# Optimization experiments

Measured on AMD Instinct MI355X. Metric: run time of the kernel, lower is better.

Reference implementation:

```python
import jax, jax.numpy as jnp
import numpy as np

B, Nq, C, H = 1, 300, 256, 8
h, w = 32, 32
HW = h * w
HID = 512  # rpe_hidden_dim
HD = C // H


def setup_inputs() -> dict:
    key = jax.random.key(0)
    ks = jax.random.split(key, 16)
    s = 0.02
    inp = {
        "raw_query": jax.random.normal(ks[0], (B, Nq, C), jnp.float32),
        "query_pos": jax.random.normal(ks[1], (B, Nq, C), jnp.float32),
        "reference_points": jax.random.uniform(ks[2], (B, Nq, 2), jnp.float32),
        "raw_src": jax.random.normal(ks[3], (B, HW, C), jnp.float32),
        "src_pos_embed": jax.random.normal(ks[4], (B, HW, C), jnp.float32),
        "Wq": jax.random.normal(ks[5], (C, C), jnp.float32) * s,
        "bq": jnp.zeros((C,), jnp.float32),
        "Wk": jax.random.normal(ks[6], (C, C), jnp.float32) * s,
        "bk": jnp.zeros((C,), jnp.float32),
        "Wv": jax.random.normal(ks[7], (C, C), jnp.float32) * s,
        "bv": jnp.zeros((C,), jnp.float32),
        "Wo": jax.random.normal(ks[8], (C, C), jnp.float32) * s,
        "bo": jnp.zeros((C,), jnp.float32),
        "W1": jax.random.normal(ks[9], (HID, 2), jnp.float32),   # cpb MLP layer 1
        "b1": jnp.zeros((HID,), jnp.float32),
        "W2": jax.random.normal(ks[10], (H, HID), jnp.float32) * s,  # cpb MLP layer 2 (no bias)
        "input_spatial_shapes": np.array([[h, w]], dtype=np.int64),
    }
    return inp


def _key_positions(hh, ww):
    ys = (jnp.arange(hh, dtype=jnp.float32) + 0.5) / hh
    xs = (jnp.arange(ww, dtype=jnp.float32) + 0.5) / ww
    yy, xx = jnp.meshgrid(ys, xs, indexing="ij")  # row-major: idx = y*w + x
    return jnp.stack([xx.ravel(), yy.ravel()], axis=-1)  # [HW, 2] (x, y)


def reference(raw_query, query_pos, reference_points, raw_src, src_pos_embed,
              Wq, bq, Wk, bk, Wv, bv, Wo, bo, W1, b1, W2, input_spatial_shapes):
    hh, ww = int(input_spatial_shapes[0, 0]), int(input_spatial_shapes[0, 1])
    scale = HD ** (-0.5)
    queries = raw_query + query_pos                      # [B,Nq,C]
    memory = raw_src + src_pos_embed                     # [B,HW,C]

    q = (queries @ Wq.T + bq).reshape(B, Nq, H, HD)
    k = (memory @ Wk.T + bk).reshape(B, hh * ww, H, HD)
    v = (memory @ Wv.T + bv).reshape(B, hh * ww, H, HD)

    logits = jnp.einsum("bqhd,bkhd->bhqk", q, k) * scale  # [B,H,Nq,HW]

    key_pos = _key_positions(hh, ww)                      # [HW,2]
    delta = reference_points[:, :, None, :] - key_pos[None, None]  # [B,Nq,HW,2]
    hid = jax.nn.relu(jnp.einsum("bqkc,hc->bqkh", delta, W1) + b1)  # [B,Nq,HW,HID]
    bias = jnp.einsum("bqkf,hf->bhqk", hid, W2)           # [B,H,Nq,HW]

    attn = jax.nn.softmax(logits + bias, axis=-1)
    out = jnp.einsum("bhqk,bkhd->bqhd", attn, v).reshape(B, Nq, C)
    return out @ Wo.T + bo
```

## Files before the change

### kernel.cpp

```cpp
#include <hip/hip_runtime.h>
#include <hip/hip_bf16.h>
#include <stdint.h>

#define NQ   300
#define CDIM 256
#define NH   8
#define HD   32
#define HWK  1024
#define HIDD 512

typedef __attribute__((ext_vector_type(8))) short short8;
typedef __attribute__((ext_vector_type(4))) float f32x4;

#define QB_OFF   0
#define KB_OFF   153600
#define VT_OFF   677888
#define PO_OFF   1202176
#define PL_OFF   3659776

__device__ __forceinline__ short sw_bf16(float x){
  union { float f; uint32_t u; } c; c.f = x;
  uint32_t u = c.u;
  u += 0x7fffu + ((u >> 16) & 1u);
  return (short)(u >> 16);
}

__device__ __forceinline__ uint32_t pk_bf16(float a, float b){
  __hip_bfloat162 h = __float22bfloat162_rn(make_float2(a, b));
  uint32_t u; __builtin_memcpy(&u, &h, 4);
  return u;
}

__global__ __launch_bounds__(256) void proj_kernel(
    const float* __restrict__ rq, const float* __restrict__ qp,
    const float* __restrict__ rs, const float* __restrict__ spe,
    const float* __restrict__ Wq, const float* __restrict__ bq,
    const float* __restrict__ Wk, const float* __restrict__ bk,
    const float* __restrict__ Wv, const float* __restrict__ bv,
    const float* __restrict__ Wo, const float* __restrict__ bo,
    char* __restrict__ ws, float* __restrict__ dout, int final_mode)
{
  int bxid = blockIdx.x;
  int tile = bxid >> 1, half = bxid & 1;
  const float *in1, *in2, *W, *bias;
  int r0, M, mode;
  const float* po = (const float*)(ws + PO_OFF);
  const float* pl = (const float*)(ws + PL_OFF);
  if (final_mode){
    in1 = po; in2 = nullptr; W = Wo; bias = bo;
    r0 = tile*16; M = NQ; mode = 3;
  } else if (tile < 19){
    in1 = rq; in2 = qp; W = Wq; bias = bq; r0 = tile*16; M = NQ; mode = 0;
  } else if (tile < 83){
    in1 = rs; in2 = spe; W = Wk; bias = bk; r0 = (tile-19)*16; M = HWK; mode = 1;
  } else {
    in1 = rs; in2 = spe; W = Wv; bias = bv; r0 = (tile-83)*16; M = HWK; mode = 2;
  }
  __shared__ __align__(16) float At[32][20];
  __shared__ float Wl[32][129];
  __shared__ float linv[16][8];
  int tid = threadIdx.x;
  int n_loc = tid & 127;
  int rg = tid >> 7;
  int n = half*128 + n_loc;
  float acc[8];
  float bv_ = bias[n];
  #pragma unroll
  for (int i=0;i<8;i++) acc[i] = bv_;

  if (mode == 3 && tid < 128){
    int r = tid >> 3, hh = tid & 7;
    int gr = r0 + r; if (gr >= M) gr = M - 1;
    float s = 0.f;
    #pragma unroll
    for (int p = 0; p < 8; p++) s += pl[((size_t)p*NQ+gr)*NH+hh];
    linv[r][hh] = 1.0f / s;
  }

  for (int c0 = 0; c0 < CDIM; c0 += 32){
    __syncthreads();
    for (int e = tid; e < 512; e += 256){
      int r = e >> 5, c = e & 31;
      int gr = r0 + r; if (gr >= M) gr = M - 1;
      float v;
      if (mode == 3){
        int cc = c0 + c;
        v = 0.f;
        #pragma unroll
        for (int p = 0; p < 8; p++) v += po[(size_t)(p*NQ+gr)*CDIM + cc];
        v *= linv[r][c0 >> 5];
      } else {
        v = in1[gr*CDIM + c0 + c];
        if (in2) v += in2[gr*CDIM + c0 + c];
      }
      At[c][r] = v;
    }
    for (int e = tid; e < 4096; e += 256){
      int c = e & 31, nn = e >> 5;
      Wl[c][nn] = W[(half*128 + nn)*CDIM + c0 + c];
    }
    __syncthreads();
    #pragma unroll
    for (int c = 0; c < 32; c++){
      float w = Wl[c][n_loc];
      const float4* ap = (const float4*)&At[c][rg*8];
      float4 a0 = ap[0], a1 = ap[1];
      acc[0] = fmaf(a0.x, w, acc[0]);
      acc[1] = fmaf(a0.y, w, acc[1]);
      acc[2] = fmaf(a0.z, w, acc[2]);
      acc[3] = fmaf(a0.w, w, acc[3]);
      acc[4] = fmaf(a1.x, w, acc[4]);
      acc[5] = fmaf(a1.y, w, acc[5]);
      acc[6] = fmaf(a1.z, w, acc[6]);
      acc[7] = fmaf(a1.w, w, acc[7]);
    }
  }

  if (mode == 0){
    short* qb = (short*)(ws + QB_OFF);
    const float s = 0.17677669529663687f;
    #pragma unroll
    for (int i=0;i<8;i++){
      int gr = r0 + rg*8 + i;
      if (gr < M) qb[gr*CDIM + n] = sw_bf16(acc[i]*s);
    }
  } else if (mode == 1){
    short* kb = (short*)(ws + KB_OFF);
    int h = n >> 5, d = n & 31;
    #pragma unroll
    for (int i=0;i<8;i++){
      int gr = r0 + rg*8 + i;
      if (gr < M) kb[((size_t)h*HWK + gr)*HD + d] = sw_bf16(acc[i]);
    }
  } else if (mode == 2){
    short* vt = (short*)(ws + VT_OFF);
    union { short8 s; uint32_t u[4]; } p;
    #pragma unroll
    for (int i=0;i<4;i++) p.u[i] = pk_bf16(acc[2*i], acc[2*i+1]);
    *(short8*)(vt + n*HWK + r0 + rg*8) = p.s;
  } else {
    #pragma unroll
    for (int i=0;i<8;i++){
      int gr = r0 + rg*8 + i;
      if (gr < M) dout[gr*CDIM + n] = acc[i];
    }
  }
}

__global__ __launch_bounds__(256, 4) void fused_kernel(
    const float* __restrict__ refp, const float* __restrict__ W1,
    const float* __restrict__ b1, const float* __restrict__ W2,
    const short* __restrict__ qb, const short* __restrict__ kb,
    const short* __restrict__ vt, float* __restrict__ po,
    float* __restrict__ pl)
{
  int bid = blockIdx.x;
  int q = bid >> 3, kr = bid & 7;
  int tid = threadIdx.x, wave = tid >> 6, lane = tid & 63;
  int n = lane & 15, qd = lane >> 4;

  __shared__ __align__(16) float wxs[HIDD];
  __shared__ __align__(16) float c1s[4][HIDD];
  __shared__ __align__(16) short w2l[NH][520];
  __shared__ __align__(16) short pb[NH][136];
  __shared__ __align__(16) float part[4][NH][32];
  __shared__ float lsum[4][NH];

  float rx = refp[2*q], ry = refp[2*q+1];
  for (int f = tid; f < HIDD; f += 256){
    float2 w = ((const float2*)W1)[f];
    wxs[f] = w.x;
    float a = fmaf(w.x, rx, fmaf(w.y, ry, b1[f]));
    #pragma unroll
    for (int r = 0; r < 4; r++){
      float ky = ((float)(kr*4 + r) + 0.5f) * (1.0f/32.0f);
      c1s[r][f] = fmaf(-w.y, ky, a);
    }
  }
  for (int e = tid; e < 512; e += 256){
    int r = e >> 6, oc = e & 63;
    const float4* p4 = (const float4*)(W2 + r*HIDD + oc*8);
    float4 x0 = p4[0], x1 = p4[1];
    union { short8 s; uint32_t u[4]; } t;
    t.u[0] = pk_bf16(x0.x, x0.y);
    t.u[1] = pk_bf16(x0.z, x0.w);
    t.u[2] = pk_bf16(x1.x, x1.y);
    t.u[3] = pk_bf16(x1.z, x1.w);
    *(short8*)&w2l[r][oc*8] = t.s;
  }
  short8 qfrag;
  if (n < NH) qfrag = *(const short8*)(qb + q*CDIM + n*HD + qd*8);
  else { short8 z = {0,0,0,0,0,0,0,0}; qfrag = z; }
  short8 qm[NH];
  #pragma unroll
  for (int h = 0; h < NH; h++){
    short8 z = {0,0,0,0,0,0,0,0};
    qm[h] = (n == h) ? qfrag : z;
  }
  __syncthreads();

  const int kyrow = kr*4 + wave;
  const int kbase = kyrow * 32;

  f32x4 acc[2];
  #pragma unroll
  for (int t = 0; t < 2; t++){
    int k0 = kbase + t*16;
    f32x4 d = {0.f,0.f,0.f,0.f};
    #pragma unroll
    for (int h = 0; h < NH; h++){
      short8 af = *(const short8*)(kb + ((size_t)h*HWK + k0 + n)*HD + qd*8);
      d = __builtin_amdgcn_mfma_f32_16x16x32_bf16(af, qm[h], d, 0, 0, 0);
    }
    acc[t] = d;
  }

  float kxA = ((float)n + 0.5f) * (1.0f/32.0f);
  float kxB = ((float)n + 16.5f) * (1.0f/32.0f);
  const float* c1r = &c1s[wave][0];
  #pragma unroll 4
  for (int kc = 0; kc < 16; kc++){
    int f0 = kc*32 + qd*8;
    f32x4 c0 = *(const f32x4*)(c1r + f0), c1v = *(const f32x4*)(c1r + f0 + 4);
    f32x4 wx0 = *(const f32x4*)&wxs[f0], wx1 = *(const f32x4*)&wxs[f0+4];
    short8 bfr = *(const short8*)&w2l[n & 7][kc*32 + qd*8];
    #pragma unroll
    for (int t = 0; t < 2; t++){
      float kx = t ? kxB : kxA;
      float e0 = fmaxf(fmaf(-wx0[0], kx, c0[0]), 0.f);
      float e1 = fmaxf(fmaf(-wx0[1], kx, c0[1]), 0.f);
      float e2 = fmaxf(fmaf(-wx0[2], kx, c0[2]), 0.f);
      float e3 = fmaxf(fmaf(-wx0[3], kx, c0[3]), 0.f);
      float e4 = fmaxf(fmaf(-wx1[0], kx, c1v[0]), 0.f);
      float e5 = fmaxf(fmaf(-wx1[1], kx, c1v[1]), 0.f);
      float e6 = fmaxf(fmaf(-wx1[2], kx, c1v[2]), 0.f);
      float e7 = fmaxf(fmaf(-wx1[3], kx, c1v[3]), 0.f);
      union { short8 s; uint32_t u[4]; } r;
      r.u[0] = pk_bf16(e0, e1);
      r.u[1] = pk_bf16(e2, e3);
      r.u[2] = pk_bf16(e4, e5);
      r.u[3] = pk_bf16(e6, e7);
      acc[t] = __builtin_amdgcn_mfma_f32_16x16x32_bf16(r.s, bfr, acc[t], 0, 0, 0);
    }
  }

  float lacc = 0.f;
  #pragma unroll
  for (int t = 0; t < 2; t++){
    float e0 = __expf(acc[t][0]);
    float e1 = __expf(acc[t][1]);
    float e2 = __expf(acc[t][2]);
    float e3 = __expf(acc[t][3]);
    if (n < NH){
      uint2 p2;
      p2.x = pk_bf16(e0, e1);
      p2.y = pk_bf16(e2, e3);
      *(uint2*)&pb[n][wave*32 + t*16 + qd*4] = p2;
    }
    float s = e0 + e1 + e2 + e3;
    s += __shfl_xor(s, 16);
    s += __shfl_xor(s, 32);
    lacc += s;
  }
  if (lane < NH) lsum[wave][lane] = lacc;

  #pragma unroll
  for (int h = 0; h < NH; h++){
    int kl = wave*32 + qd*8;
    short8 pa = *(const short8*)&pb[h][kl];
    short8 v0 = *(const short8*)(vt + ((size_t)(h*HD +      n))*HWK + kr*128 + kl);
    short8 v1 = *(const short8*)(vt + ((size_t)(h*HD + 16 + n))*HWK + kr*128 + kl);
    f32x4 o0 = {0.f,0.f,0.f,0.f}, o1 = {0.f,0.f,0.f,0.f};
    o0 = __builtin_amdgcn_mfma_f32_16x16x32_bf16(pa, v0, o0, 0, 0, 0);
    o1 = __builtin_amdgcn_mfma_f32_16x16x32_bf16(pa, v1, o1, 0, 0, 0);
    if (qd == 0){
      part[wave][h][n]      = o0[0];
      part[wave][h][16 + n] = o1[0];
    }
  }
  __syncthreads();

  {
    int h = tid >> 5, d = tid & 31;
    float s = part[0][h][d] + part[1][h][d] + part[2][h][d] + part[3][h][d];
    po[((size_t)kr*NQ + q)*CDIM + tid] = s;
    if (tid < NH)
      pl[((size_t)kr*NQ + q)*NH + tid] =
          lsum[0][tid] + lsum[1][tid] + lsum[2][tid] + lsum[3][tid];
  }
}

extern "C" void kernel_launch(void* const* d_in, const int* in_sizes, int n_in,
                              void* d_out, int out_size, void* d_ws, size_t ws_size,
                              hipStream_t stream)
{
  const float* rq  = (const float*)d_in[0];
  const float* qp  = (const float*)d_in[1];
  const float* rp  = (const float*)d_in[2];
  const float* rs  = (const float*)d_in[3];
  const float* spe = (const float*)d_in[4];
  const float* Wq  = (const float*)d_in[5];
  const float* bq  = (const float*)d_in[6];
  const float* Wk  = (const float*)d_in[7];
  const float* bk  = (const float*)d_in[8];
  const float* Wv  = (const float*)d_in[9];
  const float* bv  = (const float*)d_in[10];
  const float* Wo  = (const float*)d_in[11];
  const float* bo  = (const float*)d_in[12];
  const float* W1  = (const float*)d_in[13];
  const float* b1  = (const float*)d_in[14];
  const float* W2  = (const float*)d_in[15];
  char* ws = (char*)d_ws;
  float* dout = (float*)d_out;

  proj_kernel<<<294, 256, 0, stream>>>(rq, qp, rs, spe, Wq, bq, Wk, bk,
      Wv, bv, Wo, bo, ws, dout, 0);
  fused_kernel<<<2400, 256, 0, stream>>>(rp, W1, b1, W2,
      (const short*)(ws + QB_OFF), (const short*)(ws + KB_OFF),
      (const short*)(ws + VT_OFF), (float*)(ws + PO_OFF),
      (float*)(ws + PL_OFF));
  proj_kernel<<<38, 256, 0, stream>>>(rq, qp, rs, spe, Wq, bq, Wk, bk,
      Wv, bv, Wo, bo, ws, dout, 1);
}
```

Measured before the change: 171.5 us.

## Switch attention and RPE-MLP path from bf16 to fp16 with packed-half hidden computation

```diff
diff --git a/kernel.cpp b/kernel.cpp
--- a/kernel.cpp
+++ b/kernel.cpp
@@ -1,5 +1,5 @@
 #include <hip/hip_runtime.h>
-#include <hip/hip_bf16.h>
+#include <hip/hip_fp16.h>
 #include <stdint.h>
 
 #define NQ   300
@@ -9,7 +9,8 @@
 #define HWK  1024
 #define HIDD 512
 
-typedef __attribute__((ext_vector_type(8))) short short8;
+typedef __attribute__((ext_vector_type(8))) _Float16 f16x8;
+typedef __attribute__((ext_vector_type(2))) _Float16 h2v;
 typedef __attribute__((ext_vector_type(4))) float f32x4;
 
 #define QB_OFF   0
@@ -18,17 +19,19 @@
 #define PO_OFF   1202176
 #define PL_OFF   3659776
 
-__device__ __forceinline__ short sw_bf16(float x){
-  union { float f; uint32_t u; } c; c.f = x;
-  uint32_t u = c.u;
-  u += 0x7fffu + ((u >> 16) & 1u);
-  return (short)(u >> 16);
-}
-
-__device__ __forceinline__ uint32_t pk_bf16(float a, float b){
-  __hip_bfloat162 h = __float22bfloat162_rn(make_float2(a, b));
-  uint32_t u; __builtin_memcpy(&u, &h, 4);
-  return u;
+__device__ __forceinline__ short f16b(float x){
+  _Float16 h = (_Float16)x;
+  return __builtin_bit_cast(short, h);
+}
+
+__device__ __forceinline__ h2v cvt2h(float a, float b){
+  auto r = __builtin_amdgcn_cvt_pkrtz(a, b);
+  return __builtin_bit_cast(h2v, r);
+}
+
+__device__ __forceinline__ uint32_t pk_f16(float a, float b){
+  auto r = __builtin_amdgcn_cvt_pkrtz(a, b);
+  return __builtin_bit_cast(uint32_t, r);
 }
 
 __global__ __launch_bounds__(256) void proj_kernel(
@@ -122,7 +125,7 @@
     #pragma unroll
     for (int i=0;i<8;i++){
       int gr = r0 + rg*8 + i;
-      if (gr < M) qb[gr*CDIM + n] = sw_bf16(acc[i]*s);
+      if (gr < M) qb[gr*CDIM + n] = f16b(acc[i]*s);
     }
   } else if (mode == 1){
     short* kb = (short*)(ws + KB_OFF);
@@ -130,14 +133,14 @@
     #pragma unroll
     for (int i=0;i<8;i++){
       int gr = r0 + rg*8 + i;
-      if (gr < M) kb[((size_t)h*HWK + gr)*HD + d] = sw_bf16(acc[i]);
+      if (gr < M) kb[((size_t)h*HWK + gr)*HD + d] = f16b(acc[i]);
     }
   } else if (mode == 2){
     short* vt = (short*)(ws + VT_OFF);
-    union { short8 s; uint32_t u[4]; } p;
-    #pragma unroll
-    for (int i=0;i<4;i++) p.u[i] = pk_bf16(acc[2*i], acc[2*i+1]);
-    *(short8*)(vt + n*HWK + r0 + rg*8) = p.s;
+    uint32_t p[4];
+    #pragma unroll
+    for (int i=0;i<4;i++) p[i] = pk_f16(acc[2*i], acc[2*i+1]);
+    *(uint4*)(vt + n*HWK + r0 + rg*8) = make_uint4(p[0], p[1], p[2], p[3]);
   } else {
     #pragma unroll
     for (int i=0;i<8;i++){
@@ -159,42 +162,41 @@
   int tid = threadIdx.x, wave = tid >> 6, lane = tid & 63;
   int n = lane & 15, qd = lane >> 4;
 
-  __shared__ __align__(16) float wxs[HIDD];
-  __shared__ __align__(16) float c1s[4][HIDD];
-  __shared__ __align__(16) short w2l[NH][520];
-  __shared__ __align__(16) short pb[NH][136];
+  __shared__ __align__(16) _Float16 nwx[HIDD];
+  __shared__ __align__(16) _Float16 c1s[4][HIDD];
+  __shared__ __align__(16) _Float16 w2l[NH][520];
+  __shared__ __align__(16) _Float16 pb[NH][136];
   __shared__ __align__(16) float part[4][NH][32];
   __shared__ float lsum[4][NH];
 
   float rx = refp[2*q], ry = refp[2*q+1];
-  for (int f = tid; f < HIDD; f += 256){
-    float2 w = ((const float2*)W1)[f];
-    wxs[f] = w.x;
-    float a = fmaf(w.x, rx, fmaf(w.y, ry, b1[f]));
+  {
+    int f0 = tid * 2;
+    float4 w = *(const float4*)(W1 + 2*f0);
+    float2 bb = *(const float2*)(b1 + f0);
+    float a0 = fmaf(w.x, rx, fmaf(w.y, ry, bb.x));
+    float a1 = fmaf(w.z, rx, fmaf(w.w, ry, bb.y));
+    *(h2v*)&nwx[f0] = cvt2h(-w.x, -w.z);
     #pragma unroll
     for (int r = 0; r < 4; r++){
       float ky = ((float)(kr*4 + r) + 0.5f) * (1.0f/32.0f);
-      c1s[r][f] = fmaf(-w.y, ky, a);
-    }
-  }
-  for (int e = tid; e < 512; e += 256){
-    int r = e >> 6, oc = e & 63;
-    const float4* p4 = (const float4*)(W2 + r*HIDD + oc*8);
-    float4 x0 = p4[0], x1 = p4[1];
-    union { short8 s; uint32_t u[4]; } t;
-    t.u[0] = pk_bf16(x0.x, x0.y);
-    t.u[1] = pk_bf16(x0.z, x0.w);
-    t.u[2] = pk_bf16(x1.x, x1.y);
-    t.u[3] = pk_bf16(x1.z, x1.w);
-    *(short8*)&w2l[r][oc*8] = t.s;
-  }
-  short8 qfrag;
-  if (n < NH) qfrag = *(const short8*)(qb + q*CDIM + n*HD + qd*8);
-  else { short8 z = {0,0,0,0,0,0,0,0}; qfrag = z; }
-  short8 qm[NH];
+      float c0 = fmaf(-w.y, ky, a0);
+      float c1 = fmaf(-w.w, ky, a1);
+      *(h2v*)&c1s[r][f0] = cvt2h(c0, c1);
+    }
+  }
+  for (int e = tid; e < 2048; e += 256){
+    int r = e >> 8, j = e & 255;
+    float2 x = *(const float2*)(W2 + r*HIDD + 2*j);
+    *(h2v*)&w2l[r][2*j] = cvt2h(x.x, x.y);
+  }
+  f16x8 qfrag;
+  if (n < NH) qfrag = *(const f16x8*)(qb + q*CDIM + n*HD + qd*8);
+  else { f16x8 z = {0,0,0,0,0,0,0,0}; qfrag = z; }
+  f16x8 qm[NH];
   #pragma unroll
   for (int h = 0; h < NH; h++){
-    short8 z = {0,0,0,0,0,0,0,0};
+    f16x8 z = {0,0,0,0,0,0,0,0};
     qm[h] = (n == h) ? qfrag : z;
   }
   __syncthreads();
@@ -209,38 +211,29 @@
     f32x4 d = {0.f,0.f,0.f,0.f};
     #pragma unroll
     for (int h = 0; h < NH; h++){
-      short8 af = *(const short8*)(kb + ((size_t)h*HWK + k0 + n)*HD + qd*8);
-      d = __builtin_amdgcn_mfma_f32_16x16x32_bf16(af, qm[h], d, 0, 0, 0);
+      f16x8 af = *(const f16x8*)(kb + ((size_t)h*HWK + k0 + n)*HD + qd*8);
+      d = __builtin_amdgcn_mfma_f32_16x16x32_f16(af, qm[h], d, 0, 0, 0);
     }
     acc[t] = d;
   }
 
-  float kxA = ((float)n + 0.5f) * (1.0f/32.0f);
-  float kxB = ((float)n + 16.5f) * (1.0f/32.0f);
-  const float* c1r = &c1s[wave][0];
+  _Float16 kxAh = (_Float16)(((float)n + 0.5f) * (1.0f/32.0f));
+  _Float16 kxBh = (_Float16)(((float)n + 16.5f) * (1.0f/32.0f));
+  f16x8 kxA8, kxB8, z8;
+  #pragma unroll
+  for (int j = 0; j < 8; j++){ kxA8[j] = kxAh; kxB8[j] = kxBh; z8[j] = (_Float16)0.f; }
+  const _Float16* c1r = &c1s[wave][0];
   #pragma unroll 4
   for (int kc = 0; kc < 16; kc++){
     int f0 = kc*32 + qd*8;
-    f32x4 c0 = *(const f32x4*)(c1r + f0), c1v = *(const f32x4*)(c1r + f0 + 4);
-    f32x4 wx0 = *(const f32x4*)&wxs[f0], wx1 = *(const f32x4*)&wxs[f0+4];
-    short8 bfr = *(const short8*)&w2l[n & 7][kc*32 + qd*8];
+    f16x8 c1v = *(const f16x8*)(c1r + f0);
+    f16x8 wxv = *(const f16x8*)(&nwx[f0]);
+    f16x8 bfr = *(const f16x8*)(&w2l[n & 7][f0]);
     #pragma unroll
     for (int t = 0; t < 2; t++){
-      float kx = t ? kxB : kxA;
-      float e0 = fmaxf(fmaf(-wx0[0], kx, c0[0]), 0.f);
-      float e1 = fmaxf(fmaf(-wx0[1], kx, c0[1]), 0.f);
-      float e2 = fmaxf(fmaf(-wx0[2], kx, c0[2]), 0.f);
-      float e3 = fmaxf(fmaf(-wx0[3], kx, c0[3]), 0.f);
-      float e4 = fmaxf(fmaf(-wx1[0], kx, c1v[0]), 0.f);
-      float e5 = fmaxf(fmaf(-wx1[1], kx, c1v[1]), 0.f);
-      float e6 = fmaxf(fmaf(-wx1[2], kx, c1v[2]), 0.f);
-      float e7 = fmaxf(fmaf(-wx1[3], kx, c1v[3]), 0.f);
-      union { short8 s; uint32_t u[4]; } r;
-      r.u[0] = pk_bf16(e0, e1);
-      r.u[1] = pk_bf16(e2, e3);
-      r.u[2] = pk_bf16(e4, e5);
-      r.u[3] = pk_bf16(e6, e7);
-      acc[t] = __builtin_amdgcn_mfma_f32_16x16x32_bf16(r.s, bfr, acc[t], 0, 0, 0);
+      f16x8 kx8 = t ? kxB8 : kxA8;
+      f16x8 e = __builtin_elementwise_max(wxv * kx8 + c1v, z8);
+      acc[t] = __builtin_amdgcn_mfma_f32_16x16x32_f16(e, bfr, acc[t], 0, 0, 0);
     }
   }
 
@@ -253,8 +246,8 @@
     float e3 = __expf(acc[t][3]);
     if (n < NH){
       uint2 p2;
-      p2.x = pk_bf16(e0, e1);
-      p2.y = pk_bf16(e2, e3);
+      p2.x = pk_f16(e0, e1);
+      p2.y = pk_f16(e2, e3);
       *(uint2*)&pb[n][wave*32 + t*16 + qd*4] = p2;
     }
     float s = e0 + e1 + e2 + e3;
@@ -267,12 +260,12 @@
   #pragma unroll
   for (int h = 0; h < NH; h++){
     int kl = wave*32 + qd*8;
-    short8 pa = *(const short8*)&pb[h][kl];
-    short8 v0 = *(const short8*)(vt + ((size_t)(h*HD +      n))*HWK + kr*128 + kl);
-    short8 v1 = *(const short8*)(vt + ((size_t)(h*HD + 16 + n))*HWK + kr*128 + kl);
+    f16x8 pa = *(const f16x8*)&pb[h][kl];
+    f16x8 v0 = *(const f16x8*)(vt + ((size_t)(h*HD +      n))*HWK + kr*128 + kl);
+    f16x8 v1 = *(const f16x8*)(vt + ((size_t)(h*HD + 16 + n))*HWK + kr*128 + kl);
     f32x4 o0 = {0.f,0.f,0.f,0.f}, o1 = {0.f,0.f,0.f,0.f};
-    o0 = __builtin_amdgcn_mfma_f32_16x16x32_bf16(pa, v0, o0, 0, 0, 0);
-    o1 = __builtin_amdgcn_mfma_f32_16x16x32_bf16(pa, v1, o1, 0, 0, 0);
+    o0 = __builtin_amdgcn_mfma_f32_16x16x32_f16(pa, v0, o0, 0, 0, 0);
+    o1 = __builtin_amdgcn_mfma_f32_16x16x32_f16(pa, v1, o1, 0, 0, 0);
     if (qd == 0){
       part[wave][h][n]      = o0[0];
       part[wave][h][16 + n] = o1[0];
```

Measured after the change: 165.7 us. 1.04x faster.
